# Kernel optimization log

Measured on AMD Instinct MI355X. Metric: run time of the kernel, lower is better.

The kernel has to match this reference:

```python
import jax, jax.numpy as jnp
import numpy as np

RBF_START = 0.0
RBF_END = 8.0
RBF_STEPS = 32
OUT_SIZE = 64
ENERGY_SCALE = 0.01


def setup_inputs() -> dict:
    key = jax.random.key(0)
    k1, k2, k3, k4 = jax.random.split(key, 4)
    L, R = 512, 4096
    return {
        "lig_feat": jax.random.normal(k1, (L, RBF_STEPS, OUT_SIZE), dtype=jnp.float32),
        "rec_feat": jax.random.normal(k2, (R, RBF_STEPS, OUT_SIZE), dtype=jnp.float32),
        "lig_coord": jax.random.normal(k3, (L, 3), dtype=jnp.float32),
        "rec_coord": jax.random.normal(k4, (R, 3), dtype=jnp.float32),
    }


def reference(lig_feat, rec_feat, lig_coord, rec_coord):
    # attention coefficients: contract over (rbf step 'e' kept, feature 'f' summed)
    atn_coefs = jnp.einsum('lef,ref->lre', lig_feat, rec_feat)  # [L,R,steps]
    # pairwise distances [L,R]
    diff = lig_coord[:, None, :] - rec_coord[None, :, :]
    dists = jnp.sqrt(jnp.sum(diff * diff, axis=-1))
    # RBF encoding [L,R,steps]
    mu = jnp.linspace(RBF_START, RBF_END, RBF_STEPS, dtype=dists.dtype)
    sigma = (RBF_START - RBF_END) / RBF_STEPS
    z = (dists[..., None] - mu) / sigma
    rbfs = jnp.exp(-(z * z))
    # weighted energy sum (scalar)
    U = jnp.sum(atn_coefs * rbfs) * ENERGY_SCALE
    return U
```

## Files before the change

kernel.cpp:

```cpp
#include <hip/hip_runtime.h>
#include <math.h>

#define LN 512
#define RN 4096
#define EN 32
#define FN 64

#define BLT 128
#define BRT 128
#define EH  8

#define K16LOG2E 23.083120654223415f
#define MU_STEP (8.0f / 31.0f)

typedef _Float16 half8 __attribute__((ext_vector_type(8)));
typedef __attribute__((ext_vector_type(4))) float f32x4;

#define BUFBYTES 32768
#define BPLANE   16384

#define WS_LIG 0
#define WS_REC (2u * 1024 * 1024)
#define WS_PART (18u * 1024 * 1024)

#define LCHUNKS (LN * EN * 8)
#define RCHUNKS (RN * EN * 8)

typedef const __attribute__((address_space(1))) unsigned int* gas_ptr;
typedef __attribute__((address_space(3))) unsigned int* las_ptr;
#define GL16(g, l) __builtin_amdgcn_global_load_lds((gas_ptr)(g), (las_ptr)(l), 16, 0, 0)

__global__ __launch_bounds__(256) void ff_convert(
    const float* __restrict__ lig_feat, const float* __restrict__ rec_feat,
    unsigned short* __restrict__ lig_swz, unsigned short* __restrict__ rec_swz)
{
    int idx = blockIdx.x * 256 + threadIdx.x;
    const float* src;
    unsigned short* dst;
    if (idx < LCHUNKS) {
        src = lig_feat; dst = lig_swz;
    } else {
        idx -= LCHUNKS;
        src = rec_feat; dst = rec_swz;
    }
    const int row = idx >> 8;
    const int e   = (idx >> 3) & 31;
    const int gf  = idx & 7;

    const float* s = src + (((size_t)row * EN + e) * FN + gf * 8);
    const float4 v0 = *(const float4*)s;
    const float4 v1 = *(const float4*)(s + 4);

    const unsigned short q0 = __builtin_bit_cast(unsigned short, (_Float16)v0.x);
    const unsigned short q1 = __builtin_bit_cast(unsigned short, (_Float16)v0.y);
    const unsigned short q2 = __builtin_bit_cast(unsigned short, (_Float16)v0.z);
    const unsigned short q3 = __builtin_bit_cast(unsigned short, (_Float16)v0.w);
    const unsigned short q4 = __builtin_bit_cast(unsigned short, (_Float16)v1.x);
    const unsigned short q5 = __builtin_bit_cast(unsigned short, (_Float16)v1.y);
    const unsigned short q6 = __builtin_bit_cast(unsigned short, (_Float16)v1.z);
    const unsigned short q7 = __builtin_bit_cast(unsigned short, (_Float16)v1.w);
    uint4 o;
    o.x = (unsigned)q0 | ((unsigned)q1 << 16);
    o.y = (unsigned)q2 | ((unsigned)q3 << 16);
    o.z = (unsigned)q4 | ((unsigned)q5 << 16);
    o.w = (unsigned)q6 | ((unsigned)q7 << 16);

    const size_t dpos = (((size_t)row * EN + e) * 8 + (gf ^ (row & 7))) * 8;
    *(uint4*)(dst + dpos) = o;
}

__global__ __launch_bounds__(512, 1) void ff_mfma(
    const unsigned short* __restrict__ lig_swz,
    const unsigned short* __restrict__ rec_swz,
    const float* __restrict__ lig_coord,
    const float* __restrict__ rec_coord,
    float* __restrict__ partial)
{
    __shared__ char lds[2 * BUFBYTES];

    const int tid  = threadIdx.x;
    const int lane = tid & 63;
    const int w    = tid >> 6;
    const int wl   = (w & 3) * 2;
    const int wr   = (w >> 2) * 4;
    const int lrow = lane & 15;
    const int lk   = lane >> 4;

    const int l0 = blockIdx.y * BLT;
    const int r0 = blockIdx.x * BRT;
    const int e0 = blockIdx.z * EH;

    int soff[2];
    #pragma unroll
    for (int k = 0; k < 2; ++k) {
        const int idx = k * 512 + tid;
        soff[k] = (idx >> 3) * (EN * 128) + (idx & 7) * 16;
    }
    const char* ligb = (const char*)lig_swz + (size_t)l0 * (EN * 128);
    const char* recb = (const char*)rec_swz + (size_t)r0 * (EN * 128);

#define STAGE(b, e_) do {                                                   \
        const int ebyte_ = (e_) * 128;                                      \
        _Pragma("unroll")                                                   \
        for (int k_ = 0; k_ < 2; ++k_) {                                    \
            const int idx_ = k_ * 512 + tid;                                \
            GL16(ligb + soff[k_] + ebyte_, lds + (b) * BUFBYTES + idx_ * 16);            \
            GL16(recb + soff[k_] + ebyte_, lds + (b) * BUFBYTES + BPLANE + idx_ * 16);   \
        }                                                                   \
    } while (0)

    float rcx[4], rcy[4], rcz[4];
    #pragma unroll
    for (int tj = 0; tj < 4; ++tj) {
        const int r = r0 + (wr + tj) * 16 + lrow;
        rcx[tj] = rec_coord[r * 3 + 0];
        rcy[tj] = rec_coord[r * 3 + 1];
        rcz[tj] = rec_coord[r * 3 + 2];
    }
    float d[2][4][4];
    #pragma unroll
    for (int ti = 0; ti < 2; ++ti) {
        #pragma unroll
        for (int i = 0; i < 4; ++i) {
            const int l = l0 + (wl + ti) * 16 + lk * 4 + i;
            const float lx = lig_coord[l * 3 + 0];
            const float ly = lig_coord[l * 3 + 1];
            const float lz = lig_coord[l * 3 + 2];
            #pragma unroll
            for (int tj = 0; tj < 4; ++tj) {
                const float dx = lx - rcx[tj];
                const float dy = ly - rcy[tj];
                const float dz = lz - rcz[tj];
                d[ti][tj][i] = sqrtf(fmaf(dx, dx, fmaf(dy, dy, dz * dz)));
            }
        }
    }

    STAGE(0, e0);
    __syncthreads();

    float usum = 0.0f;

    for (int ee = 0; ee < EH; ++ee) {
        const int cur = ee & 1;
        const int e   = e0 + ee;

        if (ee + 1 < EH) STAGE(cur ^ 1, e + 1);

        const char* base = lds + cur * BUFBYTES;

        f32x4 acc[2][4];
        #pragma unroll
        for (int ti = 0; ti < 2; ++ti)
            #pragma unroll
            for (int tj = 0; tj < 4; ++tj)
                acc[ti][tj] = (f32x4){0.f, 0.f, 0.f, 0.f};

        #pragma unroll
        for (int kc = 0; kc < 2; ++kc) {
            const int inrow = (kc * 64 + lk * 16) ^ ((lrow & 7) << 4);
            half8 af[2], bf_[4];
            #pragma unroll
            for (int t = 0; t < 2; ++t) {
                const int arow = (wl + t) * 16 + lrow;
                af[t] = *(const half8*)(base + arow * 128 + inrow);
            }
            #pragma unroll
            for (int t = 0; t < 4; ++t) {
                const int brow = (wr + t) * 16 + lrow;
                bf_[t] = *(const half8*)(base + BPLANE + brow * 128 + inrow);
            }
            #pragma unroll
            for (int ti = 0; ti < 2; ++ti) {
                #pragma unroll
                for (int tj = 0; tj < 4; ++tj) {
                    acc[ti][tj] = __builtin_amdgcn_mfma_f32_16x16x32_f16(
                        af[ti], bf_[tj], acc[ti][tj], 0, 0, 0);
                }
            }
        }

        const float mu = (float)e * MU_STEP;
        #pragma unroll
        for (int ti = 0; ti < 2; ++ti) {
            #pragma unroll
            for (int tj = 0; tj < 4; ++tj) {
                #pragma unroll
                for (int i = 0; i < 4; ++i) {
                    const float t = d[ti][tj][i] - mu;
                    const float wgt = __builtin_amdgcn_exp2f(-K16LOG2E * t * t);
                    usum = fmaf(acc[ti][tj][i], wgt, usum);
                }
            }
        }

        __syncthreads();
    }

    float* red = (float*)lds;
    red[tid] = usum;
    __syncthreads();
    #pragma unroll
    for (int st = 256; st > 0; st >>= 1) {
        if (tid < st) red[tid] += red[tid + st];
        __syncthreads();
    }
    if (tid == 0) {
        const int bidx = (blockIdx.z * gridDim.y + blockIdx.y) * gridDim.x + blockIdx.x;
        partial[bidx] = red[0];
    }
#undef STAGE
}

__global__ __launch_bounds__(256) void ff_reduce(
    const float* __restrict__ partial, float* __restrict__ out, int n)
{
    __shared__ float s[256];
    float v = 0.0f;
    for (int i = threadIdx.x; i < n; i += 256) v += partial[i];
    s[threadIdx.x] = v;
    __syncthreads();
    #pragma unroll
    for (int st = 128; st > 0; st >>= 1) {
        if (threadIdx.x < st) s[threadIdx.x] += s[threadIdx.x + st];
        __syncthreads();
    }
    if (threadIdx.x == 0) out[0] = s[0] * 0.01f;
}

extern "C" void kernel_launch(void* const* d_in, const int* in_sizes, int n_in,
                              void* d_out, int out_size, void* d_ws, size_t ws_size,
                              hipStream_t stream)
{
    const float* lig_feat  = (const float*)d_in[0];
    const float* rec_feat  = (const float*)d_in[1];
    const float* lig_coord = (const float*)d_in[2];
    const float* rec_coord = (const float*)d_in[3];
    float* out = (float*)d_out;

    unsigned short* lig_swz = (unsigned short*)((char*)d_ws + WS_LIG);
    unsigned short* rec_swz = (unsigned short*)((char*)d_ws + WS_REC);
    float* partial          = (float*)((char*)d_ws + WS_PART);

    const int nChunks = LCHUNKS + RCHUNKS;
    ff_convert<<<nChunks / 256, 256, 0, stream>>>(lig_feat, rec_feat, lig_swz, rec_swz);

    const dim3 grid(RN / BRT, LN / BLT, EN / EH);
    ff_mfma<<<grid, dim3(512), 0, stream>>>(lig_swz, rec_swz, lig_coord, rec_coord, partial);

    const int nPartial = (RN / BRT) * (LN / BLT) * (EN / EH);
    ff_reduce<<<1, 256, 0, stream>>>(partial, out, nPartial);
}
```

Before: 40.02 us.

## Fuse final reduction into MFMA kernel via last-block atomic, strength-reduce RBF

Drops the separate reduce kernel launch. Each MFMA block now bumps an atomic counter that the convert kernel zeroes, and the last block to finish sums all partials and writes the output. The RBF exponent is strength-reduced into a pre-scaled offset that is decremented per step. The e-loop is fully unrolled and s_setprio is raised around the MFMA bursts. This removes one kernel launch and some VALU work, at the cost of a serial tail reduction in one block and higher register pressure from unrolling.

```diff
diff --git a/kernel.cpp b/kernel.cpp
--- a/kernel.cpp
+++ b/kernel.cpp
@@ -9,9 +9,12 @@
 #define BLT 128
 #define BRT 128
 #define EH  8
+#define NBLOCKS ((RN / BRT) * (LN / BLT) * (EN / EH))
 
 #define K16LOG2E 23.083120654223415f
-#define MU_STEP (8.0f / 31.0f)
+#define SQK      4.804489631554082f
+#define MU_STEP  (8.0f / 31.0f)
+#define SDLT     (SQK * MU_STEP)
 
 typedef _Float16 half8 __attribute__((ext_vector_type(8)));
 typedef __attribute__((ext_vector_type(4))) float f32x4;
@@ -22,6 +25,7 @@
 #define WS_LIG 0
 #define WS_REC (2u * 1024 * 1024)
 #define WS_PART (18u * 1024 * 1024)
+#define WS_CNT  (WS_PART + NBLOCKS * 4)
 
 #define LCHUNKS (LN * EN * 8)
 #define RCHUNKS (RN * EN * 8)
@@ -32,8 +36,11 @@
 
 __global__ __launch_bounds__(256) void ff_convert(
     const float* __restrict__ lig_feat, const float* __restrict__ rec_feat,
-    unsigned short* __restrict__ lig_swz, unsigned short* __restrict__ rec_swz)
+    unsigned short* __restrict__ lig_swz, unsigned short* __restrict__ rec_swz,
+    unsigned int* __restrict__ done)
 {
+    if (blockIdx.x == 0 && threadIdx.x == 0) *done = 0u;
+
     int idx = blockIdx.x * 256 + threadIdx.x;
     const float* src;
     unsigned short* dst;
@@ -74,9 +81,12 @@
     const unsigned short* __restrict__ rec_swz,
     const float* __restrict__ lig_coord,
     const float* __restrict__ rec_coord,
-    float* __restrict__ partial)
+    float* __restrict__ partial,
+    unsigned int* __restrict__ done,
+    float* __restrict__ out)
 {
     __shared__ char lds[2 * BUFBYTES];
+    __shared__ int isLast;
 
     const int tid  = threadIdx.x;
     const int lane = tid & 63;
@@ -117,7 +127,8 @@
         rcy[tj] = rec_coord[r * 3 + 1];
         rcz[tj] = rec_coord[r * 3 + 2];
     }
-    float d[2][4][4];
+    const float mu0s = -SQK * MU_STEP * (float)e0;
+    float t[2][4][4];
     #pragma unroll
     for (int ti = 0; ti < 2; ++ti) {
         #pragma unroll
@@ -131,7 +142,8 @@
                 const float dx = lx - rcx[tj];
                 const float dy = ly - rcy[tj];
                 const float dz = lz - rcz[tj];
-                d[ti][tj][i] = sqrtf(fmaf(dx, dx, fmaf(dy, dy, dz * dz)));
+                const float d = sqrtf(fmaf(dx, dx, fmaf(dy, dy, dz * dz)));
+                t[ti][tj][i] = fmaf(SQK, d, mu0s);
             }
         }
     }
@@ -141,6 +153,7 @@
 
     float usum = 0.0f;
 
+    #pragma unroll
     for (int ee = 0; ee < EH; ++ee) {
         const int cur = ee & 1;
         const int e   = e0 + ee;
@@ -161,15 +174,16 @@
             const int inrow = (kc * 64 + lk * 16) ^ ((lrow & 7) << 4);
             half8 af[2], bf_[4];
             #pragma unroll
-            for (int t = 0; t < 2; ++t) {
-                const int arow = (wl + t) * 16 + lrow;
-                af[t] = *(const half8*)(base + arow * 128 + inrow);
-            }
-            #pragma unroll
-            for (int t = 0; t < 4; ++t) {
-                const int brow = (wr + t) * 16 + lrow;
-                bf_[t] = *(const half8*)(base + BPLANE + brow * 128 + inrow);
-            }
+            for (int tt = 0; tt < 2; ++tt) {
+                const int arow = (wl + tt) * 16 + lrow;
+                af[tt] = *(const half8*)(base + arow * 128 + inrow);
+            }
+            #pragma unroll
+            for (int tt = 0; tt < 4; ++tt) {
+                const int brow = (wr + tt) * 16 + lrow;
+                bf_[tt] = *(const half8*)(base + BPLANE + brow * 128 + inrow);
+            }
+            __builtin_amdgcn_s_setprio(1);
             #pragma unroll
             for (int ti = 0; ti < 2; ++ti) {
                 #pragma unroll
@@ -178,18 +192,19 @@
                         af[ti], bf_[tj], acc[ti][tj], 0, 0, 0);
                 }
             }
-        }
-
-        const float mu = (float)e * MU_STEP;
+            __builtin_amdgcn_s_setprio(0);
+        }
+
         #pragma unroll
         for (int ti = 0; ti < 2; ++ti) {
             #pragma unroll
             for (int tj = 0; tj < 4; ++tj) {
                 #pragma unroll
                 for (int i = 0; i < 4; ++i) {
-                    const float t = d[ti][tj][i] - mu;
-                    const float wgt = __builtin_amdgcn_exp2f(-K16LOG2E * t * t);
+                    const float u = t[ti][tj][i] * t[ti][tj][i];
+                    const float wgt = __builtin_amdgcn_exp2f(-u);
                     usum = fmaf(acc[ti][tj][i], wgt, usum);
+                    t[ti][tj][i] -= SDLT;
                 }
             }
         }
@@ -205,27 +220,26 @@
         if (tid < st) red[tid] += red[tid + st];
         __syncthreads();
     }
+
+    const int bidx = (blockIdx.z * gridDim.y + blockIdx.y) * gridDim.x + blockIdx.x;
     if (tid == 0) {
-        const int bidx = (blockIdx.z * gridDim.y + blockIdx.y) * gridDim.x + blockIdx.x;
         partial[bidx] = red[0];
+        __threadfence();
+        isLast = (atomicAdd(done, 1u) == NBLOCKS - 1u);
+    }
+    __syncthreads();
+    if (isLast) {
+        __threadfence();
+        red[tid] = partial[tid];
+        __syncthreads();
+        #pragma unroll
+        for (int st = 256; st > 0; st >>= 1) {
+            if (tid < st) red[tid] += red[tid + st];
+            __syncthreads();
+        }
+        if (tid == 0) out[0] = red[0] * 0.01f;
     }
 #undef STAGE
-}
-
-__global__ __launch_bounds__(256) void ff_reduce(
-    const float* __restrict__ partial, float* __restrict__ out, int n)
-{
-    __shared__ float s[256];
-    float v = 0.0f;
-    for (int i = threadIdx.x; i < n; i += 256) v += partial[i];
-    s[threadIdx.x] = v;
-    __syncthreads();
-    #pragma unroll
-    for (int st = 128; st > 0; st >>= 1) {
-        if (threadIdx.x < st) s[threadIdx.x] += s[threadIdx.x + st];
-        __syncthreads();
-    }
-    if (threadIdx.x == 0) out[0] = s[0] * 0.01f;
 }
 
 extern "C" void kernel_launch(void* const* d_in, const int* in_sizes, int n_in,
@@ -241,13 +255,12 @@
     unsigned short* lig_swz = (unsigned short*)((char*)d_ws + WS_LIG);
     unsigned short* rec_swz = (unsigned short*)((char*)d_ws + WS_REC);
     float* partial          = (float*)((char*)d_ws + WS_PART);
+    unsigned int* done      = (unsigned int*)((char*)d_ws + WS_CNT);
 
     const int nChunks = LCHUNKS + RCHUNKS;
-    ff_convert<<<nChunks / 256, 256, 0, stream>>>(lig_feat, rec_feat, lig_swz, rec_swz);
+    ff_convert<<<nChunks / 256, 256, 0, stream>>>(lig_feat, rec_feat, lig_swz, rec_swz, done);
 
     const dim3 grid(RN / BRT, LN / BLT, EN / EH);
-    ff_mfma<<<grid, dim3(512), 0, stream>>>(lig_swz, rec_swz, lig_coord, rec_coord, partial);
-
-    const int nPartial = (RN / BRT) * (LN / BLT) * (EN / EH);
-    ff_reduce<<<1, 256, 0, stream>>>(partial, out, nPartial);
+    ff_mfma<<<grid, dim3(512), 0, stream>>>(lig_swz, rec_swz, lig_coord, rec_coord,
+                                            partial, done, out);
 }
```

Result: slower. 48.12 us (+20.2%).
